# Optimization experiments

Measured on AMD Instinct MI355X. Metric: run time of the kernel, lower is better.

## Reference

```python
import jax, jax.numpy as jnp
import numpy as np

B, N, D = 4, 2048, 1024

def setup_inputs() -> dict:
    key = jax.random.key(0)
    ks = jax.random.split(key, 8)
    s = 1.0 / np.sqrt(D)
    return {
        "x": jax.random.normal(ks[0], (B, N, D), dtype=jnp.float32),
        "Wq": jax.random.normal(ks[1], (D, D), dtype=jnp.float32) * s,
        "bq": jnp.zeros((D,), dtype=jnp.float32),
        "Wk": jax.random.normal(ks[2], (D, D), dtype=jnp.float32) * s,
        "bk": jnp.zeros((D,), dtype=jnp.float32),
        "Wv": jax.random.normal(ks[3], (D, D), dtype=jnp.float32) * s,
        "bv": jnp.zeros((D,), dtype=jnp.float32),
        "gamma": jnp.ones((1,), dtype=jnp.float32),
    }

def reference(x, Wq, bq, Wk, bk, Wv, bv, gamma):
    d = x.shape[-1]
    delta = 1.0 / jnp.sqrt(jnp.asarray(d, dtype=x.dtype))
    # torch Linear: y = x @ W.T + b, W is [out, in]
    Q = jnp.einsum('bnd,ed->bne', x, Wq) + bq
    K = jnp.einsum('bnd,ed->bne', x, Wk) + bk
    V = jnp.einsum('bnd,ed->bne', x, Wv) + bv
    scores = jnp.einsum('bne,bme->bnm', Q, K) * delta  # [B, N, N]
    attn = jax.nn.softmax(scores, axis=-1)
    out = jnp.einsum('bnm,bme->bne', attn, V)
    return out * gamma + x
```

## Files before the change

### kernel.cpp

```cpp
#include <hip/hip_runtime.h>

typedef _Float16 f16;
typedef __attribute__((ext_vector_type(4))) _Float16 f16x4;
typedef __attribute__((ext_vector_type(8))) _Float16 f16x8;
typedef __attribute__((ext_vector_type(4))) float f32x4;

#define B_ 4
#define N_ 2048
#define D_ 1024

__global__ __launch_bounds__(256) void k_cast_all(const float4* __restrict__ x,
                                                  const float4* __restrict__ wq,
                                                  const float4* __restrict__ wk,
                                                  const float4* __restrict__ wv,
                                                  f16x4* __restrict__ xo,
                                                  f16x4* __restrict__ wqo,
                                                  f16x4* __restrict__ wko,
                                                  f16x4* __restrict__ wvo,
                                                  float* __restrict__ rowsum) {
  int b = blockIdx.x;
  if (b >= 11264) {
    rowsum[(b - 11264) * 256 + threadIdx.x] = 0.f;
    return;
  }
  const float4* in;
  f16x4* out;
  int idx;
  if (b < 8192)       { in = x;  out = xo;  idx = b * 256 + threadIdx.x; }
  else if (b < 9216)  { in = wq; out = wqo; idx = (b - 8192) * 256 + threadIdx.x; }
  else if (b < 10240) { in = wk; out = wko; idx = (b - 9216) * 256 + threadIdx.x; }
  else                { in = wv; out = wvo; idx = (b - 10240) * 256 + threadIdx.x; }
  float4 v = in[idx];
  f16x4 o = { (_Float16)v.x, (_Float16)v.y, (_Float16)v.z, (_Float16)v.w };
  out[idx] = o;
}

__device__ __forceinline__ void stage_tile(const char* gRowBase, int rowStrideBytes,
                                           int kByte, char* lds, int tid) {
#pragma unroll
  for (int it = 0; it < 4; ++it) {
    int lin = it * 4096 + tid * 16;
    int row = lin >> 7;
    int pchunk = (lin >> 4) & 7;
    int lchunk = pchunk ^ (row & 7);
    const char* g = gRowBase + (long)row * rowStrideBytes + kByte + lchunk * 16;
    char* l = lds + it * 4096 + ((tid >> 6) << 10);
    __builtin_amdgcn_global_load_lds(
        (const __attribute__((address_space(1))) unsigned int*)g,
        (__attribute__((address_space(3))) unsigned int*)l, 16, 0, 0);
  }
}

__device__ __forceinline__ void gemm_mainloop(const f16* __restrict__ A, int lda,
                                              const f16* __restrict__ B, int ldb,
                                              int K, char* ldsA, char* ldsB,
                                              f32x4 acc[4][4]) {
  const int tid = threadIdx.x;
  const int lane = tid & 63, wave = tid >> 6;
  const int wm = wave >> 1, wn = wave & 1;
  const int quad = lane >> 4, l16 = lane & 15;
  const char* Ab = (const char*)A;
  const char* Bb = (const char*)B;
  const int nK = K >> 6;
  for (int ks = 0; ks < nK; ++ks) {
    __syncthreads();
    stage_tile(Ab, lda * 2, ks * 128, ldsA, tid);
    stage_tile(Bb, ldb * 2, ks * 128, ldsB, tid);
    __syncthreads();
#pragma unroll
    for (int kk = 0; kk < 2; ++kk) {
      f16x8 af[4], bfv[4];
#pragma unroll
      for (int i = 0; i < 4; ++i) {
        int c = kk * 4 + quad;
        int rA = wm * 64 + i * 16 + l16;
        af[i] = *(const f16x8*)(ldsA + rA * 128 + ((c ^ (rA & 7)) << 4));
        int rB = wn * 64 + i * 16 + l16;
        bfv[i] = *(const f16x8*)(ldsB + rB * 128 + ((c ^ (rB & 7)) << 4));
      }
#pragma unroll
      for (int i = 0; i < 4; ++i)
#pragma unroll
        for (int j = 0; j < 4; ++j)
          acc[i][j] = __builtin_amdgcn_mfma_f32_16x16x32_f16(af[i], bfv[j], acc[i][j], 0, 0, 0);
    }
  }
}

__global__ __launch_bounds__(256, 2) void k_qkv(const f16* __restrict__ X,
                                                const f16* __restrict__ Wq,
                                                const f16* __restrict__ Wk,
                                                const f16* __restrict__ Wv,
                                                const float* __restrict__ bq,
                                                const float* __restrict__ bk,
                                                const float* __restrict__ bv,
                                                f16* __restrict__ Q, f16* __restrict__ Ko,
                                                f16* __restrict__ Vt) {
  __shared__ __align__(16) char lds[65536];
  char* ldsX = lds;
  int fid = blockIdx.x + 8 * blockIdx.y;
  int c_ = fid & 7, k_ = fid >> 3;
  int lx = k_ & 7;
  int ly = c_ * 8 + (k_ >> 3);
  int tm = ly * 128, tn = lx * 128;
  const int tid = threadIdx.x;
  const int lane = tid & 63, wave = tid >> 6;
  const int wm = wave >> 1, wn = wave & 1;
  const int quad = lane >> 4, l16 = lane & 15;
  f32x4 acc[3][4][4];
#pragma unroll
  for (int w = 0; w < 3; ++w)
#pragma unroll
    for (int i = 0; i < 4; ++i)
#pragma unroll
      for (int j = 0; j < 4; ++j) acc[w][i][j] = (f32x4){0.f, 0.f, 0.f, 0.f};

  const char* Xb = (const char*)(X + (long)tm * D_);
  const char* Wb[3] = { (const char*)(Wq + (long)tn * D_),
                        (const char*)(Wk + (long)tn * D_),
                        (const char*)(Wv + (long)tn * D_) };
  for (int ks = 0; ks < (D_ >> 6); ++ks) {
    __syncthreads();
    stage_tile(Xb, D_ * 2, ks * 128, ldsX, tid);
#pragma unroll
    for (int w = 0; w < 3; ++w) stage_tile(Wb[w], D_ * 2, ks * 128, lds + 16384 * (w + 1), tid);
    __syncthreads();
#pragma unroll
    for (int kk = 0; kk < 2; ++kk) {
      f16x8 af[4];
#pragma unroll
      for (int i = 0; i < 4; ++i) {
        int c = kk * 4 + quad;
        int rA = wm * 64 + i * 16 + l16;
        af[i] = *(const f16x8*)(ldsX + rA * 128 + ((c ^ (rA & 7)) << 4));
      }
#pragma unroll
      for (int w = 0; w < 3; ++w) {
        f16x8 bfv[4];
#pragma unroll
        for (int j = 0; j < 4; ++j) {
          int c = kk * 4 + quad;
          int rB = wn * 64 + j * 16 + l16;
          bfv[j] = *(const f16x8*)(lds + 16384 * (w + 1) + rB * 128 + ((c ^ (rB & 7)) << 4));
        }
#pragma unroll
        for (int i = 0; i < 4; ++i)
#pragma unroll
          for (int j = 0; j < 4; ++j)
            acc[w][i][j] = __builtin_amdgcn_mfma_f32_16x16x32_f16(af[i], bfv[j], acc[w][i][j], 0, 0, 0);
      }
    }
  }

  const float* biases[2] = { bq, bk };
  f16* outs[2] = { Q, Ko };
#pragma unroll
  for (int w = 0; w < 2; ++w) {
    f16* out = outs[w];
#pragma unroll
    for (int j = 0; j < 4; ++j) {
      int col = tn + wn * 64 + j * 16 + l16;
      float bb = biases[w][col];
#pragma unroll
      for (int i = 0; i < 4; ++i) {
        int rbase = tm + wm * 64 + i * 16 + quad * 4;
#pragma unroll
        for (int r = 0; r < 4; ++r)
          out[(long)(rbase + r) * D_ + col] = (_Float16)(acc[w][i][j][r] + bb);
      }
    }
  }

  __syncthreads();
  f16* ldsT = (f16*)lds;
#pragma unroll
  for (int j = 0; j < 4; ++j) {
    int cl = wn * 64 + j * 16 + l16;
    float bb = bv[tn + cl];
#pragma unroll
    for (int i = 0; i < 4; ++i) {
      int rl = wm * 64 + i * 16 + quad * 4;
      f16x4 p = { (_Float16)(acc[2][i][j][0] + bb), (_Float16)(acc[2][i][j][1] + bb),
                  (_Float16)(acc[2][i][j][2] + bb), (_Float16)(acc[2][i][j][3] + bb) };
      *(f16x4*)(ldsT + cl * 136 + rl) = p;
    }
  }
  __syncthreads();
  int bb_ = tm >> 11, nbase = tm & 2047;
  f16* VtB = Vt + (long)bb_ * D_ * N_ + nbase;
#pragma unroll
  for (int it = 0; it < 8; ++it) {
    int f = it * 16 + (tid >> 4);
    int c = tid & 15;
    f16x8 v = *(const f16x8*)(ldsT + f * 136 + c * 8);
    *(f16x8*)(VtB + (long)(tn + f) * N_ + c * 8) = v;
  }
}

__global__ __launch_bounds__(256) void k_scores(const f16* __restrict__ Q,
                                                const f16* __restrict__ Kf,
                                                f16* __restrict__ S,
                                                float* __restrict__ rowsum) {
  __shared__ __align__(16) char lds[36864];
  int b = blockIdx.z;
  int fid = blockIdx.x + 16 * blockIdx.y;
  int c_ = fid & 7, k_ = fid >> 3;
  int lx = 4 * (c_ & 3) + (k_ & 3);
  int ly = 8 * (c_ >> 2) + (k_ >> 2);
  int tm = ly * 128, tn = lx * 128;
  const f16* A = Q + (long)b * N_ * D_ + (long)tm * D_;
  const f16* Bm = Kf + (long)b * N_ * D_ + (long)tn * D_;
  f32x4 acc[4][4];
#pragma unroll
  for (int i = 0; i < 4; ++i)
#pragma unroll
    for (int j = 0; j < 4; ++j) acc[i][j] = (f32x4){0.f, 0.f, 0.f, 0.f};
  gemm_mainloop(A, D_, Bm, D_, D_, lds, lds + 16384, acc);
  f16* Sb = S + (long)b * N_ * N_;
  const float delta = 0.03125f;
  int tid = threadIdx.x, lane = tid & 63, wave = tid >> 6;
  int wm = wave >> 1, wn = wave & 1, quad = lane >> 4, l16 = lane & 15;

  __syncthreads();
  f16* ldsS = (f16*)lds;
  float rsum[4][4];
#pragma unroll
  for (int i = 0; i < 4; ++i)
#pragma unroll
    for (int r = 0; r < 4; ++r) rsum[i][r] = 0.f;
#pragma unroll
  for (int j = 0; j < 4; ++j) {
    int col = wn * 64 + j * 16 + l16;
#pragma unroll
    for (int i = 0; i < 4; ++i) {
      int rbase = wm * 64 + i * 16 + quad * 4;
#pragma unroll
      for (int r = 0; r < 4; ++r) {
        float e = __expf(acc[i][j][r] * delta);
        rsum[i][r] += e;
        ldsS[(rbase + r) * 136 + col] = (_Float16)e;
      }
    }
  }
#pragma unroll
  for (int m = 1; m < 16; m <<= 1)
#pragma unroll
    for (int i = 0; i < 4; ++i)
#pragma unroll
      for (int r = 0; r < 4; ++r) rsum[i][r] += __shfl_xor(rsum[i][r], m);
  if (l16 == 0) {
    float* rs = rowsum + (long)b * N_ + tm;
#pragma unroll
    for (int i = 0; i < 4; ++i)
#pragma unroll
      for (int r = 0; r < 4; ++r)
        atomicAdd(rs + wm * 64 + i * 16 + quad * 4 + r, rsum[i][r]);
  }
  __syncthreads();
  int rloc = tid >> 4, c = tid & 15;
#pragma unroll
  for (int p = 0; p < 8; ++p) {
    int row = p * 16 + rloc;
    f16x8 v = *(const f16x8*)((const char*)ldsS + row * 272 + c * 16);
    *(f16x8*)(Sb + (long)(tm + row) * N_ + tn + c * 8) = v;
  }
}

__global__ __launch_bounds__(256) void k_out(const f16* __restrict__ P,
                                             const f16* __restrict__ Vt,
                                             const f16* __restrict__ xf,
                                             const float* __restrict__ gamma,
                                             const float* __restrict__ rowsum,
                                             float* __restrict__ out) {
  __shared__ __align__(16) char ldsA[16384];
  __shared__ __align__(16) char ldsB[16384];
  int b = blockIdx.z;
  int fid = blockIdx.x + 8 * blockIdx.y;
  int c_ = fid & 7, k_ = fid >> 3;
  int lx = 4 * (c_ & 1) + (k_ & 3);
  int ly = 4 * (c_ >> 1) + (k_ >> 2);
  int tm = ly * 128, tn = lx * 128;
  const f16* A = P + (long)b * N_ * N_ + (long)tm * N_;
  const f16* Bm = Vt + (long)b * D_ * N_ + (long)tn * N_;
  f32x4 acc[4][4];
#pragma unroll
  for (int i = 0; i < 4; ++i)
#pragma unroll
    for (int j = 0; j < 4; ++j) acc[i][j] = (f32x4){0.f, 0.f, 0.f, 0.f};
  gemm_mainloop(A, N_, Bm, N_, N_, ldsA, ldsB, acc);
  float g = gamma[0];
  int tid = threadIdx.x, lane = tid & 63, wave = tid >> 6;
  int wm = wave >> 1, wn = wave & 1, quad = lane >> 4, l16 = lane & 15;
  float inv[4][4];
#pragma unroll
  for (int i = 0; i < 4; ++i)
#pragma unroll
    for (int r = 0; r < 4; ++r)
      inv[i][r] = g / rowsum[(long)b * N_ + tm + wm * 64 + i * 16 + quad * 4 + r];
#pragma unroll
  for (int j = 0; j < 4; ++j) {
    int col = tn + wn * 64 + j * 16 + l16;
#pragma unroll
    for (int i = 0; i < 4; ++i) {
      int rbase = tm + wm * 64 + i * 16 + quad * 4;
#pragma unroll
      for (int r = 0; r < 4; ++r) {
        long idx = (long)b * N_ * D_ + (long)(rbase + r) * D_ + col;
        out[idx] = acc[i][j][r] * inv[i][r] + (float)xf[idx];
      }
    }
  }
}

extern "C" void kernel_launch(void* const* d_in, const int* in_sizes, int n_in,
                              void* d_out, int out_size, void* d_ws, size_t ws_size,
                              hipStream_t stream) {
  const float* x  = (const float*)d_in[0];
  const float* Wq = (const float*)d_in[1];
  const float* bq = (const float*)d_in[2];
  const float* Wk = (const float*)d_in[3];
  const float* bk = (const float*)d_in[4];
  const float* Wv = (const float*)d_in[5];
  const float* bv = (const float*)d_in[6];
  const float* gamma = (const float*)d_in[7];
  float* out = (float*)d_out;
  char* ws = (char*)d_ws;

  f16* Qb  = (f16*)(ws);
  f16* Kb  = (f16*)(ws + (16u << 20));
  f16* Vt  = (f16*)(ws + (32u << 20));
  f16* Xb  = (f16*)(ws + (48u << 20));
  f16* Wqb = (f16*)(ws + (64u << 20));
  f16* Wkb = (f16*)(ws + (66u << 20));
  f16* Wvb = (f16*)(ws + (68u << 20));
  f16* S   = (f16*)(ws + (64u << 20));
  float* rowsum = (float*)(ws + (96u << 20));

  k_cast_all<<<11296, 256, 0, stream>>>((const float4*)x, (const float4*)Wq,
                                        (const float4*)Wk, (const float4*)Wv,
                                        (f16x4*)Xb, (f16x4*)Wqb, (f16x4*)Wkb, (f16x4*)Wvb,
                                        rowsum);
  k_qkv<<<dim3(8, 64), 256, 0, stream>>>(Xb, Wqb, Wkb, Wvb, bq, bk, bv, Qb, Kb, Vt);
  k_scores<<<dim3(16, 16, 4), 256, 0, stream>>>(Qb, Kb, S, rowsum);
  k_out<<<dim3(8, 16, 4), 256, 0, stream>>>(S, Vt, Xb, gamma, rowsum, out);
}
```

Measured before the change: 263.3 us.

## Fuse scores and output GEMMs into one kernel with per-row-block flags

Result: slower. 495.1 us (+88.1%).

```diff
diff --git a/kernel.cpp b/kernel.cpp
--- a/kernel.cpp
+++ b/kernel.cpp
@@ -17,10 +17,11 @@
                                                   f16x4* __restrict__ wqo,
                                                   f16x4* __restrict__ wko,
                                                   f16x4* __restrict__ wvo,
-                                                  float* __restrict__ rowsum) {
+                                                  int* __restrict__ zero8256) {
   int b = blockIdx.x;
   if (b >= 11264) {
-    rowsum[(b - 11264) * 256 + threadIdx.x] = 0.f;
+    int i = (b - 11264) * 256 + threadIdx.x;
+    if (i < 8256) zero8256[i] = 0;
     return;
   }
   const float4* in;
@@ -197,116 +198,124 @@
   }
 }
 
-__global__ __launch_bounds__(256) void k_scores(const f16* __restrict__ Q,
-                                                const f16* __restrict__ Kf,
-                                                f16* __restrict__ S,
-                                                float* __restrict__ rowsum) {
+__global__ __launch_bounds__(256) void k_attn(const f16* __restrict__ Q,
+                                              const f16* __restrict__ Kf,
+                                              f16* __restrict__ S,
+                                              const f16* __restrict__ Vt,
+                                              const f16* __restrict__ xf,
+                                              const float* __restrict__ gamma,
+                                              float* __restrict__ rowsum,
+                                              int* __restrict__ flags,
+                                              float* __restrict__ out) {
   __shared__ __align__(16) char lds[36864];
-  int b = blockIdx.z;
-  int fid = blockIdx.x + 16 * blockIdx.y;
-  int c_ = fid & 7, k_ = fid >> 3;
-  int lx = 4 * (c_ & 3) + (k_ & 3);
-  int ly = 8 * (c_ >> 2) + (k_ >> 2);
-  int tm = ly * 128, tn = lx * 128;
-  const f16* A = Q + (long)b * N_ * D_ + (long)tm * D_;
-  const f16* Bm = Kf + (long)b * N_ * D_ + (long)tn * D_;
-  f32x4 acc[4][4];
-#pragma unroll
-  for (int i = 0; i < 4; ++i)
-#pragma unroll
-    for (int j = 0; j < 4; ++j) acc[i][j] = (f32x4){0.f, 0.f, 0.f, 0.f};
-  gemm_mainloop(A, D_, Bm, D_, D_, lds, lds + 16384, acc);
-  f16* Sb = S + (long)b * N_ * N_;
-  const float delta = 0.03125f;
-  int tid = threadIdx.x, lane = tid & 63, wave = tid >> 6;
-  int wm = wave >> 1, wn = wave & 1, quad = lane >> 4, l16 = lane & 15;
-
-  __syncthreads();
-  f16* ldsS = (f16*)lds;
-  float rsum[4][4];
-#pragma unroll
-  for (int i = 0; i < 4; ++i)
-#pragma unroll
-    for (int r = 0; r < 4; ++r) rsum[i][r] = 0.f;
-#pragma unroll
-  for (int j = 0; j < 4; ++j) {
-    int col = wn * 64 + j * 16 + l16;
-#pragma unroll
-    for (int i = 0; i < 4; ++i) {
-      int rbase = wm * 64 + i * 16 + quad * 4;
-#pragma unroll
-      for (int r = 0; r < 4; ++r) {
-        float e = __expf(acc[i][j][r] * delta);
-        rsum[i][r] += e;
-        ldsS[(rbase + r) * 136 + col] = (_Float16)e;
-      }
-    }
-  }
-#pragma unroll
-  for (int m = 1; m < 16; m <<= 1)
-#pragma unroll
-    for (int i = 0; i < 4; ++i)
-#pragma unroll
-      for (int r = 0; r < 4; ++r) rsum[i][r] += __shfl_xor(rsum[i][r], m);
-  if (l16 == 0) {
-    float* rs = rowsum + (long)b * N_ + tm;
+  const int tid = threadIdx.x;
+  const int lane = tid & 63, wave = tid >> 6;
+  const int wm = wave >> 1, wn = wave & 1;
+  const int quad = lane >> 4, l16 = lane & 15;
+  const int bid = blockIdx.x;
+
+  {
+    int b = bid >> 8, f = bid & 255;
+    int c_ = f & 7, k_ = f >> 3;
+    int lx = 4 * (c_ & 3) + (k_ & 3);
+    int ly = 8 * (c_ >> 2) + (k_ >> 2);
+    int tm = ly * 128, tn = lx * 128;
+    const f16* A = Q + (long)b * N_ * D_ + (long)tm * D_;
+    const f16* Bm = Kf + (long)b * N_ * D_ + (long)tn * D_;
+    f32x4 acc[4][4];
+#pragma unroll
+    for (int i = 0; i < 4; ++i)
+#pragma unroll
+      for (int j = 0; j < 4; ++j) acc[i][j] = (f32x4){0.f, 0.f, 0.f, 0.f};
+    gemm_mainloop(A, D_, Bm, D_, D_, lds, lds + 16384, acc);
+    f16* Sb = S + (long)b * N_ * N_;
+    const float delta = 0.03125f;
+
+    __syncthreads();
+    f16* ldsS = (f16*)lds;
+    float rsum[4][4];
+#pragma unroll
+    for (int i = 0; i < 4; ++i)
+#pragma unroll
+      for (int r = 0; r < 4; ++r) rsum[i][r] = 0.f;
+#pragma unroll
+    for (int j = 0; j < 4; ++j) {
+      int col = wn * 64 + j * 16 + l16;
+#pragma unroll
+      for (int i = 0; i < 4; ++i) {
+        int rbase = wm * 64 + i * 16 + quad * 4;
+#pragma unroll
+        for (int r = 0; r < 4; ++r) {
+          float e = __expf(acc[i][j][r] * delta);
+          rsum[i][r] += e;
+          ldsS[(rbase + r) * 136 + col] = (_Float16)e;
+        }
+      }
+    }
+#pragma unroll
+    for (int m = 1; m < 16; m <<= 1)
+#pragma unroll
+      for (int i = 0; i < 4; ++i)
+#pragma unroll
+        for (int r = 0; r < 4; ++r) rsum[i][r] += __shfl_xor(rsum[i][r], m);
+    if (l16 == 0) {
+      float* rs = rowsum + (long)b * N_ + tm;
+#pragma unroll
+      for (int i = 0; i < 4; ++i)
+#pragma unroll
+        for (int r = 0; r < 4; ++r)
+          atomicAdd(rs + wm * 64 + i * 16 + quad * 4 + r, rsum[i][r]);
+    }
+    __syncthreads();
+    int rloc = tid >> 4, c = tid & 15;
+#pragma unroll
+    for (int p = 0; p < 8; ++p) {
+      int row = p * 16 + rloc;
+      f16x8 v = *(const f16x8*)((const char*)ldsS + row * 272 + c * 16);
+      *(f16x8*)(Sb + (long)(tm + row) * N_ + tn + c * 8) = v;
+    }
+    __threadfence();
+    __syncthreads();
+    if (tid == 0) atomicAdd(flags + b * 16 + ly, 1);
+  }
+
+  if (bid < 512) {
+    int b2 = bid >> 7, f2 = bid & 127;
+    int c2 = f2 & 7, k2 = f2 >> 3;
+    int lx2 = 4 * (c2 & 1) + (k2 & 3);
+    int ly2 = 4 * (c2 >> 1) + (k2 >> 2);
+    int tm = ly2 * 128, tn = lx2 * 128;
+    if (tid == 0) {
+      while (atomicAdd(flags + b2 * 16 + ly2, 0) < 16) __builtin_amdgcn_s_sleep(2);
+    }
+    __syncthreads();
+    __threadfence();
+    const f16* A = S + (long)b2 * N_ * N_ + (long)tm * N_;
+    const f16* Bm = Vt + (long)b2 * D_ * N_ + (long)tn * N_;
+    f32x4 acc[4][4];
+#pragma unroll
+    for (int i = 0; i < 4; ++i)
+#pragma unroll
+      for (int j = 0; j < 4; ++j) acc[i][j] = (f32x4){0.f, 0.f, 0.f, 0.f};
+    gemm_mainloop(A, N_, Bm, N_, N_, lds, lds + 16384, acc);
+    float g = gamma[0];
+    float inv[4][4];
 #pragma unroll
     for (int i = 0; i < 4; ++i)
 #pragma unroll
       for (int r = 0; r < 4; ++r)
-        atomicAdd(rs + wm * 64 + i * 16 + quad * 4 + r, rsum[i][r]);
-  }
-  __syncthreads();
-  int rloc = tid >> 4, c = tid & 15;
-#pragma unroll
-  for (int p = 0; p < 8; ++p) {
-    int row = p * 16 + rloc;
-    f16x8 v = *(const f16x8*)((const char*)ldsS + row * 272 + c * 16);
-    *(f16x8*)(Sb + (long)(tm + row) * N_ + tn + c * 8) = v;
-  }
-}
-
-__global__ __launch_bounds__(256) void k_out(const f16* __restrict__ P,
-                                             const f16* __restrict__ Vt,
-                                             const f16* __restrict__ xf,
-                                             const float* __restrict__ gamma,
-                                             const float* __restrict__ rowsum,
-                                             float* __restrict__ out) {
-  __shared__ __align__(16) char ldsA[16384];
-  __shared__ __align__(16) char ldsB[16384];
-  int b = blockIdx.z;
-  int fid = blockIdx.x + 8 * blockIdx.y;
-  int c_ = fid & 7, k_ = fid >> 3;
-  int lx = 4 * (c_ & 1) + (k_ & 3);
-  int ly = 4 * (c_ >> 1) + (k_ >> 2);
-  int tm = ly * 128, tn = lx * 128;
-  const f16* A = P + (long)b * N_ * N_ + (long)tm * N_;
-  const f16* Bm = Vt + (long)b * D_ * N_ + (long)tn * N_;
-  f32x4 acc[4][4];
-#pragma unroll
-  for (int i = 0; i < 4; ++i)
-#pragma unroll
-    for (int j = 0; j < 4; ++j) acc[i][j] = (f32x4){0.f, 0.f, 0.f, 0.f};
-  gemm_mainloop(A, N_, Bm, N_, N_, ldsA, ldsB, acc);
-  float g = gamma[0];
-  int tid = threadIdx.x, lane = tid & 63, wave = tid >> 6;
-  int wm = wave >> 1, wn = wave & 1, quad = lane >> 4, l16 = lane & 15;
-  float inv[4][4];
-#pragma unroll
-  for (int i = 0; i < 4; ++i)
-#pragma unroll
-    for (int r = 0; r < 4; ++r)
-      inv[i][r] = g / rowsum[(long)b * N_ + tm + wm * 64 + i * 16 + quad * 4 + r];
-#pragma unroll
-  for (int j = 0; j < 4; ++j) {
-    int col = tn + wn * 64 + j * 16 + l16;
-#pragma unroll
-    for (int i = 0; i < 4; ++i) {
-      int rbase = tm + wm * 64 + i * 16 + quad * 4;
-#pragma unroll
-      for (int r = 0; r < 4; ++r) {
-        long idx = (long)b * N_ * D_ + (long)(rbase + r) * D_ + col;
-        out[idx] = acc[i][j][r] * inv[i][r] + (float)xf[idx];
+        inv[i][r] = g / rowsum[(long)b2 * N_ + tm + wm * 64 + i * 16 + quad * 4 + r];
+#pragma unroll
+    for (int j = 0; j < 4; ++j) {
+      int col = tn + wn * 64 + j * 16 + l16;
+#pragma unroll
+      for (int i = 0; i < 4; ++i) {
+        int rbase = tm + wm * 64 + i * 16 + quad * 4;
+#pragma unroll
+        for (int r = 0; r < 4; ++r) {
+          long idx = (long)b2 * N_ * D_ + (long)(rbase + r) * D_ + col;
+          out[idx] = acc[i][j][r] * inv[i][r] + (float)xf[idx];
+        }
       }
     }
   }
@@ -333,14 +342,15 @@
   f16* Wqb = (f16*)(ws + (64u << 20));
   f16* Wkb = (f16*)(ws + (66u << 20));
   f16* Wvb = (f16*)(ws + (68u << 20));
-  f16* S   = (f16*)(ws + (64u << 20));
-  float* rowsum = (float*)(ws + (96u << 20));
-
-  k_cast_all<<<11296, 256, 0, stream>>>((const float4*)x, (const float4*)Wq,
+  size_t sOff = (ws_size >= (140ull << 20)) ? (96ull << 20) : (64ull << 20);
+  f16* S = (f16*)(ws + sOff);
+  float* rowsum = (float*)(ws + sOff + (32ull << 20));
+  int* flags = (int*)((char*)rowsum + 8192 * 4);
+
+  k_cast_all<<<11297, 256, 0, stream>>>((const float4*)x, (const float4*)Wq,
                                         (const float4*)Wk, (const float4*)Wv,
                                         (f16x4*)Xb, (f16x4*)Wqb, (f16x4*)Wkb, (f16x4*)Wvb,
-                                        rowsum);
+                                        (int*)rowsum);
   k_qkv<<<dim3(8, 64), 256, 0, stream>>>(Xb, Wqb, Wkb, Wvb, bq, bk, bv, Qb, Kb, Vt);
-  k_scores<<<dim3(16, 16, 4), 256, 0, stream>>>(Qb, Kb, S, rowsum);
-  k_out<<<dim3(8, 16, 4), 256, 0, stream>>>(S, Vt, Xb, gamma, rowsum, out);
-}
+  k_attn<<<1024, 256, 0, stream>>>(Qb, Kb, S, Vt, Xb, gamma, rowsum, flags, out);
+}
```

## Quantize QKV projection inputs to FP8 and use scaled MFMA 16x16x128

Applied to the files above, without the earlier changes.

New measurement: 263.2 us. No clear change (-0.0%).

```diff
diff --git a/kernel.cpp b/kernel.cpp
--- a/kernel.cpp
+++ b/kernel.cpp
@@ -4,6 +4,8 @@
 typedef __attribute__((ext_vector_type(4))) _Float16 f16x4;
 typedef __attribute__((ext_vector_type(8))) _Float16 f16x8;
 typedef __attribute__((ext_vector_type(4))) float f32x4;
+typedef __attribute__((ext_vector_type(4))) int i32x4;
+typedef __attribute__((ext_vector_type(8))) int i32x8;
 
 #define B_ 4
 #define N_ 2048
@@ -13,10 +15,10 @@
                                                   const float4* __restrict__ wq,
                                                   const float4* __restrict__ wk,
                                                   const float4* __restrict__ wv,
-                                                  f16x4* __restrict__ xo,
-                                                  f16x4* __restrict__ wqo,
-                                                  f16x4* __restrict__ wko,
-                                                  f16x4* __restrict__ wvo,
+                                                  int* __restrict__ xo,
+                                                  int* __restrict__ wqo,
+                                                  int* __restrict__ wko,
+                                                  int* __restrict__ wvo,
                                                   float* __restrict__ rowsum) {
   int b = blockIdx.x;
   if (b >= 11264) {
@@ -24,15 +26,17 @@
     return;
   }
   const float4* in;
-  f16x4* out;
+  int* out;
   int idx;
-  if (b < 8192)       { in = x;  out = xo;  idx = b * 256 + threadIdx.x; }
-  else if (b < 9216)  { in = wq; out = wqo; idx = (b - 8192) * 256 + threadIdx.x; }
-  else if (b < 10240) { in = wk; out = wko; idx = (b - 9216) * 256 + threadIdx.x; }
-  else                { in = wv; out = wvo; idx = (b - 10240) * 256 + threadIdx.x; }
+  float s;
+  if (b < 8192)       { in = x;  out = xo;  idx = b * 256 + threadIdx.x; s = 1.f; }
+  else if (b < 9216)  { in = wq; out = wqo; idx = (b - 8192) * 256 + threadIdx.x; s = 32.f; }
+  else if (b < 10240) { in = wk; out = wko; idx = (b - 9216) * 256 + threadIdx.x; s = 32.f; }
+  else                { in = wv; out = wvo; idx = (b - 10240) * 256 + threadIdx.x; s = 32.f; }
   float4 v = in[idx];
-  f16x4 o = { (_Float16)v.x, (_Float16)v.y, (_Float16)v.z, (_Float16)v.w };
-  out[idx] = o;
+  int w = __builtin_amdgcn_cvt_pk_fp8_f32(v.x * s, v.y * s, 0, false);
+  w = __builtin_amdgcn_cvt_pk_fp8_f32(v.z * s, v.w * s, w, true);
+  out[idx] = w;
 }
 
 __device__ __forceinline__ void stage_tile(const char* gRowBase, int rowStrideBytes,
@@ -49,6 +53,14 @@
         (const __attribute__((address_space(1))) unsigned int*)g,
         (__attribute__((address_space(3))) unsigned int*)l, 16, 0, 0);
   }
+}
+
+__device__ __forceinline__ i32x8 frag8(const char* lds, int row, int quad) {
+  int c0 = (2 * quad) ^ (row & 7);
+  int c1 = (2 * quad + 1) ^ (row & 7);
+  i32x4 lo = *(const i32x4*)(lds + row * 128 + (c0 << 4));
+  i32x4 hi = *(const i32x4*)(lds + row * 128 + (c1 << 4));
+  return (i32x8){lo.x, lo.y, lo.z, lo.w, hi.x, hi.y, hi.z, hi.w};
 }
 
 __device__ __forceinline__ void gemm_mainloop(const f16* __restrict__ A, int lda,
@@ -87,10 +99,10 @@
   }
 }
 
-__global__ __launch_bounds__(256, 2) void k_qkv(const f16* __restrict__ X,
-                                                const f16* __restrict__ Wq,
-                                                const f16* __restrict__ Wk,
-                                                const f16* __restrict__ Wv,
+__global__ __launch_bounds__(256, 2) void k_qkv(const char* __restrict__ X8,
+                                                const char* __restrict__ Wq8,
+                                                const char* __restrict__ Wk8,
+                                                const char* __restrict__ Wv8,
                                                 const float* __restrict__ bq,
                                                 const float* __restrict__ bk,
                                                 const float* __restrict__ bv,
@@ -115,43 +127,34 @@
 #pragma unroll
       for (int j = 0; j < 4; ++j) acc[w][i][j] = (f32x4){0.f, 0.f, 0.f, 0.f};
 
-  const char* Xb = (const char*)(X + (long)tm * D_);
-  const char* Wb[3] = { (const char*)(Wq + (long)tn * D_),
-                        (const char*)(Wk + (long)tn * D_),
-                        (const char*)(Wv + (long)tn * D_) };
-  for (int ks = 0; ks < (D_ >> 6); ++ks) {
+  const char* Xb = X8 + (long)tm * D_;
+  const char* Wb[3] = { Wq8 + (long)tn * D_, Wk8 + (long)tn * D_, Wv8 + (long)tn * D_ };
+  const int idScale = 0x7F7F7F7F;
+  for (int ks = 0; ks < (D_ >> 7); ++ks) {
     __syncthreads();
-    stage_tile(Xb, D_ * 2, ks * 128, ldsX, tid);
-#pragma unroll
-    for (int w = 0; w < 3; ++w) stage_tile(Wb[w], D_ * 2, ks * 128, lds + 16384 * (w + 1), tid);
+    stage_tile(Xb, D_, ks * 128, ldsX, tid);
+#pragma unroll
+    for (int w = 0; w < 3; ++w) stage_tile(Wb[w], D_, ks * 128, lds + 16384 * (w + 1), tid);
     __syncthreads();
-#pragma unroll
-    for (int kk = 0; kk < 2; ++kk) {
-      f16x8 af[4];
-#pragma unroll
-      for (int i = 0; i < 4; ++i) {
-        int c = kk * 4 + quad;
-        int rA = wm * 64 + i * 16 + l16;
-        af[i] = *(const f16x8*)(ldsX + rA * 128 + ((c ^ (rA & 7)) << 4));
-      }
-#pragma unroll
-      for (int w = 0; w < 3; ++w) {
-        f16x8 bfv[4];
-#pragma unroll
-        for (int j = 0; j < 4; ++j) {
-          int c = kk * 4 + quad;
-          int rB = wn * 64 + j * 16 + l16;
-          bfv[j] = *(const f16x8*)(lds + 16384 * (w + 1) + rB * 128 + ((c ^ (rB & 7)) << 4));
-        }
+    i32x8 af[4];
+#pragma unroll
+    for (int i = 0; i < 4; ++i)
+      af[i] = frag8(ldsX, wm * 64 + i * 16 + l16, quad);
+#pragma unroll
+    for (int w = 0; w < 3; ++w) {
+      const char* ldsW = lds + 16384 * (w + 1);
+#pragma unroll
+      for (int j = 0; j < 4; ++j) {
+        i32x8 bf = frag8(ldsW, wn * 64 + j * 16 + l16, quad);
 #pragma unroll
         for (int i = 0; i < 4; ++i)
-#pragma unroll
-          for (int j = 0; j < 4; ++j)
-            acc[w][i][j] = __builtin_amdgcn_mfma_f32_16x16x32_f16(af[i], bfv[j], acc[w][i][j], 0, 0, 0);
-      }
-    }
-  }
-
+          acc[w][i][j] = __builtin_amdgcn_mfma_scale_f32_16x16x128_f8f6f4(
+              af[i], bf, acc[w][i][j], 0, 0, 0, idScale, 0, idScale);
+      }
+    }
+  }
+
+  const float wuns = 0.03125f;
   const float* biases[2] = { bq, bk };
   f16* outs[2] = { Q, Ko };
 #pragma unroll
@@ -166,7 +169,7 @@
         int rbase = tm + wm * 64 + i * 16 + quad * 4;
 #pragma unroll
         for (int r = 0; r < 4; ++r)
-          out[(long)(rbase + r) * D_ + col] = (_Float16)(acc[w][i][j][r] + bb);
+          out[(long)(rbase + r) * D_ + col] = (_Float16)(acc[w][i][j][r] * wuns + bb);
       }
     }
   }
@@ -180,8 +183,8 @@
 #pragma unroll
     for (int i = 0; i < 4; ++i) {
       int rl = wm * 64 + i * 16 + quad * 4;
-      f16x4 p = { (_Float16)(acc[2][i][j][0] + bb), (_Float16)(acc[2][i][j][1] + bb),
-                  (_Float16)(acc[2][i][j][2] + bb), (_Float16)(acc[2][i][j][3] + bb) };
+      f16x4 p = { (_Float16)(acc[2][i][j][0] * wuns + bb), (_Float16)(acc[2][i][j][1] * wuns + bb),
+                  (_Float16)(acc[2][i][j][2] * wuns + bb), (_Float16)(acc[2][i][j][3] * wuns + bb) };
       *(f16x4*)(ldsT + cl * 136 + rl) = p;
     }
   }
@@ -268,7 +271,7 @@
 
 __global__ __launch_bounds__(256) void k_out(const f16* __restrict__ P,
                                              const f16* __restrict__ Vt,
-                                             const f16* __restrict__ xf,
+                                             const float* __restrict__ x,
                                              const float* __restrict__ gamma,
                                              const float* __restrict__ rowsum,
                                              float* __restrict__ out) {
@@ -306,7 +309,7 @@
 #pragma unroll
       for (int r = 0; r < 4; ++r) {
         long idx = (long)b * N_ * D_ + (long)(rbase + r) * D_ + col;
-        out[idx] = acc[i][j][r] * inv[i][r] + (float)xf[idx];
+        out[idx] = acc[i][j][r] * inv[i][r] + x[idx];
       }
     }
   }
@@ -329,18 +332,18 @@
   f16* Qb  = (f16*)(ws);
   f16* Kb  = (f16*)(ws + (16u << 20));
   f16* Vt  = (f16*)(ws + (32u << 20));
-  f16* Xb  = (f16*)(ws + (48u << 20));
-  f16* Wqb = (f16*)(ws + (64u << 20));
-  f16* Wkb = (f16*)(ws + (66u << 20));
-  f16* Wvb = (f16*)(ws + (68u << 20));
+  char* X8  = ws + (48u << 20);
+  char* Wq8 = ws + (56u << 20);
+  char* Wk8 = ws + (57u << 20);
+  char* Wv8 = ws + (58u << 20);
   f16* S   = (f16*)(ws + (64u << 20));
   float* rowsum = (float*)(ws + (96u << 20));
 
   k_cast_all<<<11296, 256, 0, stream>>>((const float4*)x, (const float4*)Wq,
                                         (const float4*)Wk, (const float4*)Wv,
-                                        (f16x4*)Xb, (f16x4*)Wqb, (f16x4*)Wkb, (f16x4*)Wvb,
+                                        (int*)X8, (int*)Wq8, (int*)Wk8, (int*)Wv8,
                                         rowsum);
-  k_qkv<<<dim3(8, 64), 256, 0, stream>>>(Xb, Wqb, Wkb, Wvb, bq, bk, bv, Qb, Kb, Vt);
+  k_qkv<<<dim3(8, 64), 256, 0, stream>>>(X8, Wq8, Wk8, Wv8, bq, bk, bv, Qb, Kb, Vt);
   k_scores<<<dim3(16, 16, 4), 256, 0, stream>>>(Qb, Kb, S, rowsum);
-  k_out<<<dim3(8, 16, 4), 256, 0, stream>>>(S, Vt, Xb, gamma, rowsum, out);
-}
+  k_out<<<dim3(8, 16, 4), 256, 0, stream>>>(S, Vt, x, gamma, rowsum, out);
+}
```
